# Kernel optimization log

Measured on AMD Instinct MI355X. Metric: run time of the kernel, lower is better.

## Reference

```python
import jax, jax.numpy as jnp
import numpy as np

CH = [32, 64, 128, 256, 512]
# per decoder stage s (s=0 deepest): conv_a Cin = CH[3-s] + in_ch, Cout = CH[3-s]; conv_b CH[3-s]->CH[3-s]
STAGE_DIMS = [(768, 256), (384, 128), (192, 64), (96, 32)]


def three_interpolation(p1, p2, x2):
    """p1 [B,N1,3] dense coords, p2 [B,N2,3] sparse coords, x2 [B,C,N2] -> [B,C,N1]."""
    d2 = (jnp.sum(p1 * p1, -1)[:, :, None]
          - 2.0 * jnp.einsum('bnd,bmd->bnm', p1, p2)
          + jnp.sum(p2 * p2, -1)[:, None, :])            # [B,N1,N2] squared dists
    neg_d, idx = jax.lax.top_k(-d2, 3)                   # 3 nearest neighbors
    dist = jnp.maximum(-neg_d, 0.0)                      # [B,N1,3]
    w = 1.0 / (dist + 1e-8)
    w = w / jnp.sum(w, axis=-1, keepdims=True)           # inverse-distance weights
    gathered = jax.vmap(lambda x, i: x[:, i])(x2, idx)   # [B,C,N1,3]
    return jnp.einsum('bcnk,bnk->bcn', gathered, w)


def conv_bn_relu(x, W, g, b):
    # 1x1 conv1d + BN (eval: running mean 0, var 1) + ReLU
    y = jnp.einsum('oc,bcn->bon', W, x)
    return jax.nn.relu(y * g[None, :, None] + b[None, :, None])


def setup_inputs() -> dict:
    key = jax.random.key(0)
    B = 8
    Ns = [8192, 2048, 512, 128, 32]
    inp = {}
    keys = jax.random.split(key, 64)
    ki = 0
    for i, n in enumerate(Ns):
        inp[f'p{i}'] = jax.random.uniform(keys[ki], (B, n, 3), jnp.float32); ki += 1
        inp[f'f{i}'] = jax.random.normal(keys[ki], (B, CH[i], n), jnp.float32); ki += 1
    for s, (cin, cout) in enumerate(STAGE_DIMS):
        inp[f'w{s}a'] = jax.random.normal(keys[ki], (cout, cin), jnp.float32) * 0.05; ki += 1
        inp[f'g{s}a'] = 1.0 + 0.1 * jax.random.normal(keys[ki], (cout,), jnp.float32); ki += 1
        inp[f'b{s}a'] = 0.1 * jax.random.normal(keys[ki], (cout,), jnp.float32); ki += 1
        inp[f'w{s}b'] = jax.random.normal(keys[ki], (cout, cout), jnp.float32) * 0.05; ki += 1
        inp[f'g{s}b'] = 1.0 + 0.1 * jax.random.normal(keys[ki], (cout,), jnp.float32); ki += 1
        inp[f'b{s}b'] = 0.1 * jax.random.normal(keys[ki], (cout,), jnp.float32); ki += 1
    return inp


def reference(p0, p1, p2, p3, p4, f0, f1, f2, f3, f4,
              w0a, g0a, b0a, w0b, g0b, b0b,
              w1a, g1a, b1a, w1b, g1b, b1b,
              w2a, g2a, b2a, w2b, g2b, b2b,
              w3a, g3a, b3a, w3b, g3b, b3b):
    p = [p0, p1, p2, p3, p4]
    f = [f0, f1, f2, f3, f4]
    params = [(w0a, g0a, b0a, w0b, g0b, b0b),
              (w1a, g1a, b1a, w1b, g1b, b1b),
              (w2a, g2a, b2a, w2b, g2b, b2b),
              (w3a, g3a, b3a, w3b, g3b, b3b)]
    # decoder stage s propagates level (4-s) -> (3-s)
    for s in range(4):
        lvl = 3 - s
        interp = three_interpolation(p[lvl], p[lvl + 1], f[lvl + 1])
        x = jnp.concatenate([f[lvl], interp], axis=1)
        wa, ga, ba, wb, gb, bb = params[s]
        x = conv_bn_relu(x, wa, ga, ba)
        x = conv_bn_relu(x, wb, gb, bb)
        f[lvl] = x
    return f[0]
```

## Files before the change

kernel.cpp:

```cpp
#include <hip/hip_runtime.h>

#define KNN_INF 3.0e38f
#define GD 8
#define NCELL 512
#define H 0.125f


__global__ __launch_bounds__(512) void bin_kernel(const float* __restrict__ p2,
                                                  float4* __restrict__ bpts,
                                                  int* __restrict__ bidx,
                                                  int* __restrict__ cstart,
                                                  int N2) {
    __shared__ int cnt[NCELL], cnt0[NCELL], cur[NCELL];
    __shared__ int cellof[2048];
    int b = blockIdx.x;
    int t = threadIdx.x;
    cnt[t] = 0;
    __syncthreads();
    float xs[4], ys[4], zs[4];
    for (int i = 0; i < 4; ++i) {
        int m = t * 4 + i;
        const float* q = p2 + ((size_t)b * N2 + m) * 3;
        float x = q[0], y = q[1], z = q[2];
        xs[i] = x; ys[i] = y; zs[i] = z;
        int ix = min(GD - 1, max(0, (int)(x * 8.0f)));
        int iy = min(GD - 1, max(0, (int)(y * 8.0f)));
        int iz = min(GD - 1, max(0, (int)(z * 8.0f)));
        int c = (ix << 6) | (iy << 3) | iz;
        cellof[m] = c;
        atomicAdd(&cnt[c], 1);
    }
    __syncthreads();
    int myc = cnt[t];
    cnt0[t] = myc;
    __syncthreads();
    for (int off = 1; off < NCELL; off <<= 1) {
        int v = (t >= off) ? cnt[t - off] : 0;
        __syncthreads();
        cnt[t] += v;
        __syncthreads();
    }
    int excl = cnt[t] - cnt0[t];
    cur[t] = excl;
    cstart[b * (NCELL + 1) + t] = excl;
    if (t == 0) cstart[b * (NCELL + 1) + NCELL] = N2;
    __syncthreads();
    for (int i = 0; i < 4; ++i) {
        int m = t * 4 + i;
        int c = cellof[m];
        int pos = atomicAdd(&cur[c], 1);
        float x = xs[i], y = ys[i], z = zs[i];
        bpts[(size_t)b * N2 + pos] = make_float4(x, y, z, x * x + y * y + z * z);
        bidx[(size_t)b * N2 + pos] = m;
    }
}

__device__ __forceinline__ bool lex_lt(float da, int ia, float db, int ib) {
    return (da < db) || (da == db && ia < ib);
}

__global__ __launch_bounds__(256) void knn_query_kernel(
    const float* __restrict__ p1,
    const float4* __restrict__ bpts,
    const int* __restrict__ bidx,
    const int* __restrict__ cstart,
    int* __restrict__ idx, float* __restrict__ w,
    int N1, int N2) {
    int n = blockIdx.x * 256 + threadIdx.x;
    int b = blockIdx.y;
    if (n >= N1) return;
    const float* pp = p1 + ((size_t)b * N1 + n) * 3;
    float px = pp[0], py = pp[1], pz = pp[2];
    float s1 = px * px + py * py + pz * pz;
    int cx = min(GD - 1, max(0, (int)(px * 8.0f)));
    int cy = min(GD - 1, max(0, (int)(py * 8.0f)));
    int cz = min(GD - 1, max(0, (int)(pz * 8.0f)));
    float d0 = KNN_INF, d1 = KNN_INF, d2 = KNN_INF;
    int i0 = 0, i1 = 0, i2 = 0;
    const float4* bp = bpts + (size_t)b * N2;
    const int* bi = bidx + (size_t)b * N2;
    const int* cs = cstart + b * (NCELL + 1);

#define SCAN_CELL(ci, cj, ck)                                            \
    {                                                                    \
        int c_ = ((ci) << 6) | ((cj) << 3) | (ck);                       \
        int e_ = cs[c_ + 1];                                             \
        for (int m_ = cs[c_]; m_ < e_; ++m_) {                           \
            float4 q = bp[m_];                                           \
            int om = bi[m_];                                             \
            float dot = px * q.x + py * q.y + pz * q.z;                  \
            float d = fmaf(-2.0f, dot, s1 + q.w);                        \
            if (lex_lt(d, om, d2, i2)) {                                 \
                if (lex_lt(d, om, d1, i1)) {                             \
                    d2 = d1; i2 = i1;                                    \
                    if (lex_lt(d, om, d0, i0)) {                         \
                        d1 = d0; i1 = i0; d0 = d; i0 = om;               \
                    } else { d1 = d; i1 = om; }                          \
                } else { d2 = d; i2 = om; }                              \
            }                                                            \
        }                                                                \
    }

    int x0 = max(cx - 1, 0), x1 = min(cx + 1, GD - 1);
    int y0 = max(cy - 1, 0), y1 = min(cy + 1, GD - 1);
    int z0 = max(cz - 1, 0), z1 = min(cz + 1, GD - 1);
    for (int i = x0; i <= x1; ++i)
        for (int j = y0; j <= y1; ++j)
            for (int k = z0; k <= z1; ++k)
                SCAN_CELL(i, j, k);

    int r = 1;
    while (true) {
        float mL = (cx - r > 0)      ? (px - (float)(cx - r) * H)     : KNN_INF;
        float mR = (cx + r < GD - 1) ? ((float)(cx + r + 1) * H - px) : KNN_INF;
        float mD = (cy - r > 0)      ? (py - (float)(cy - r) * H)     : KNN_INF;
        float mU = (cy + r < GD - 1) ? ((float)(cy + r + 1) * H - py) : KNN_INF;
        float mB = (cz - r > 0)      ? (pz - (float)(cz - r) * H)     : KNN_INF;
        float mF = (cz + r < GD - 1) ? ((float)(cz + r + 1) * H - pz) : KNN_INF;
        float mg = fminf(fminf(fminf(mL, mR), fminf(mD, mU)), fminf(mB, mF));
        if (mg >= 1.0e18f) break;
        if (d2 <= mg * mg * 0.99999f) break;
        int nx0 = max(cx - r - 1, 0), nx1 = min(cx + r + 1, GD - 1);
        int ny0 = max(cy - r - 1, 0), ny1 = min(cy + r + 1, GD - 1);
        int nz0 = max(cz - r - 1, 0), nz1 = min(cz + r + 1, GD - 1);
        for (int i = nx0; i <= nx1; ++i)
            for (int j = ny0; j <= ny1; ++j)
                for (int k = nz0; k <= nz1; ++k) {
                    if (i >= x0 && i <= x1 && j >= y0 && j <= y1 && k >= z0 && k <= z1)
                        continue;
                    SCAN_CELL(i, j, k);
                }
        x0 = nx0; x1 = nx1; y0 = ny0; y1 = ny1; z0 = nz0; z1 = nz1;
        ++r;
    }
#undef SCAN_CELL

    float dd0 = fmaxf(d0, 0.0f), dd1 = fmaxf(d1, 0.0f), dd2 = fmaxf(d2, 0.0f);
    float w0 = 1.0f / (dd0 + 1e-8f);
    float w1 = 1.0f / (dd1 + 1e-8f);
    float w2 = 1.0f / (dd2 + 1e-8f);
    float wsum = w0 + w1 + w2;
    w0 /= wsum; w1 /= wsum; w2 /= wsum;
    size_t ob = ((size_t)b * N1 + n) * 3;
    idx[ob + 0] = i0; idx[ob + 1] = i1; idx[ob + 2] = i2;
    w[ob + 0] = w0; w[ob + 1] = w1; w[ob + 2] = w2;
}

struct KnnAll {
    const float* p1[3]; const float* p2[3];
    float* pd[3]; int* pi[3];
    int N1[3], N2[3], chunk[3], nchunk[3], nbx[3];
    int bs1, bs2;
};

__global__ void knn_all_kernel(KnnAll P) {
    __shared__ float4 sm4[256];
    int bid = blockIdx.x;
    int s = (bid >= P.bs1) + (bid >= P.bs2);
    int start = (s == 0) ? 0 : (s == 1) ? P.bs1 : P.bs2;
    int local = bid - start;
    int nbx = P.nbx[s];
    int bx = local % nbx;
    int rest = local / nbx;
    int b = rest & 7;
    int z = rest >> 3;
    int N1 = P.N1[s], N2 = P.N2[s], chunk = P.chunk[s], nchunk = P.nchunk[s];
    int m0 = z * chunk;
    const float* p2b = P.p2[s] + ((size_t)b * N2 + m0) * 3;
    for (int m = threadIdx.x; m < chunk; m += blockDim.x) {
        float x = p2b[m * 3 + 0], y = p2b[m * 3 + 1], zz = p2b[m * 3 + 2];
        sm4[m] = make_float4(x, y, zz, x * x + y * y + zz * zz);
    }
    __syncthreads();
    int n = bx * blockDim.x + threadIdx.x;
    if (n >= N1) return;
    const float* p1b = P.p1[s] + ((size_t)b * N1 + n) * 3;
    float px = p1b[0], py = p1b[1], pz = p1b[2];
    float s1 = px * px + py * py + pz * pz;
    float d0 = KNN_INF, d1 = KNN_INF, d2 = KNN_INF;
    int i0 = 0, i1 = 0, i2 = 0;
    for (int m = 0; m < chunk; ++m) {
        float4 q = sm4[m];
        float dot = px * q.x + py * q.y + pz * q.z;
        float d = fmaf(-2.0f, dot, s1 + q.w);
        if (d < d2) {
            if (d < d1) {
                d2 = d1; i2 = i1;
                if (d < d0) { d1 = d0; i1 = i0; d0 = d; i0 = m; }
                else        { d1 = d;  i1 = m; }
            } else { d2 = d; i2 = m; }
        }
    }
    size_t base = (((size_t)b * N1 + n) * nchunk + z) * 3;
    float* pd = P.pd[s]; int* pi = P.pi[s];
    pd[base + 0] = d0; pd[base + 1] = d1; pd[base + 2] = d2;
    pi[base + 0] = m0 + i0; pi[base + 1] = m0 + i1; pi[base + 2] = m0 + i2;
}

struct MergeAll {
    const float* pd[3]; const int* pi[3];
    int* idx[3]; float* w[3];
    int nchunk[3];
    int ts1, ts2;
};

__global__ void knn_merge_all_kernel(MergeAll P, int total) {
    int t = blockIdx.x * blockDim.x + threadIdx.x;
    if (t >= total) return;
    int s = (t >= P.ts1) + (t >= P.ts2);
    int start = (s == 0) ? 0 : (s == 1) ? P.ts1 : P.ts2;
    int lt = t - start;
    int nchunk = P.nchunk[s];
    float d0 = KNN_INF, d1 = KNN_INF, d2 = KNN_INF;
    int i0 = 0, i1 = 0, i2 = 0;
    const float* pd = P.pd[s]; const int* pi = P.pi[s];
    size_t base = (size_t)lt * nchunk * 3;
    for (int c = 0; c < nchunk * 3; ++c) {
        float d = pd[base + c];
        int   i = pi[base + c];
        if (d < d2) {
            if (d < d1) {
                d2 = d1; i2 = i1;
                if (d < d0) { d1 = d0; i1 = i0; d0 = d; i0 = i; }
                else        { d1 = d;  i1 = i; }
            } else { d2 = d; i2 = i; }
        }
    }
    float dd0 = fmaxf(d0, 0.0f), dd1 = fmaxf(d1, 0.0f), dd2 = fmaxf(d2, 0.0f);
    float w0 = 1.0f / (dd0 + 1e-8f);
    float w1 = 1.0f / (dd1 + 1e-8f);
    float w2 = 1.0f / (dd2 + 1e-8f);
    float wsum = w0 + w1 + w2;
    w0 /= wsum; w1 /= wsum; w2 /= wsum;
    size_t ob = (size_t)lt * 3;
    P.idx[s][ob + 0] = i0; P.idx[s][ob + 1] = i1; P.idx[s][ob + 2] = i2;
    P.w[s][ob + 0] = w0; P.w[s][ob + 1] = w1; P.w[s][ob + 2] = w2;
}

#define TO 32
#define TN 64
#define BK 16
template<bool PARTIAL>
__global__ __launch_bounds__(256) void conv_a_fused_kernel(
    const float* __restrict__ f1, const float* __restrict__ x2,
    const int* __restrict__ idxS, const float* __restrict__ wS,
    const float* __restrict__ W, const float* __restrict__ g, const float* __restrict__ bv,
    float* __restrict__ Y,
    int C1, int C2, int N, int N2, int Cout, int chunk) {
    __shared__ float Ws[BK][TO];
    __shared__ float Xs[BK][TN];
    int Cin = C1 + C2;
    int zb = blockIdx.z;
    int b = zb & 7;
    int split = zb >> 3;
    int kBase = split * chunk;
    int oBase = blockIdx.y * TO;
    int nBase = blockIdx.x * TN;
    int tid = threadIdx.x;
    int tx = tid & 15;
    int ty = tid >> 4;
    int nn = tid & 63;
    int kk0 = tid >> 6;
    int n = nBase + nn;
    size_t gb = ((size_t)b * N + n) * 3;
    int j0 = idxS[gb + 0], j1 = idxS[gb + 1], j2 = idxS[gb + 2];
    float w0g = wS[gb + 0], w1g = wS[gb + 1], w2g = wS[gb + 2];
    const float* f1b = f1 + (size_t)b * C1 * N;
    const float* x2b = x2 + (size_t)b * C2 * N2;
    float acc[2][4] = {{0.f, 0.f, 0.f, 0.f}, {0.f, 0.f, 0.f, 0.f}};
    for (int k0 = kBase; k0 < kBase + chunk; k0 += BK) {
        for (int t = tid; t < TO * BK; t += 256) {
            int o = t / BK, kk = t % BK;
            Ws[kk][o] = W[(size_t)(oBase + o) * Cin + k0 + kk];
        }
#pragma unroll
        for (int i = 0; i < 4; ++i) {
            int kk = kk0 + i * 4;
            int k = k0 + kk;
            float v;
            if (k < C1) {
                v = f1b[(size_t)k * N + n];
            } else {
                const float* r = x2b + (size_t)(k - C1) * N2;
                v = r[j0] * w0g + r[j1] * w1g + r[j2] * w2g;
            }
            Xs[kk][nn] = v;
        }
        __syncthreads();
#pragma unroll
        for (int kk = 0; kk < BK; ++kk) {
            float w0 = Ws[kk][ty * 2 + 0];
            float w1 = Ws[kk][ty * 2 + 1];
            float4 xv = *reinterpret_cast<const float4*>(&Xs[kk][tx * 4]);
            acc[0][0] = fmaf(w0, xv.x, acc[0][0]);
            acc[0][1] = fmaf(w0, xv.y, acc[0][1]);
            acc[0][2] = fmaf(w0, xv.z, acc[0][2]);
            acc[0][3] = fmaf(w0, xv.w, acc[0][3]);
            acc[1][0] = fmaf(w1, xv.x, acc[1][0]);
            acc[1][1] = fmaf(w1, xv.y, acc[1][1]);
            acc[1][2] = fmaf(w1, xv.z, acc[1][2]);
            acc[1][3] = fmaf(w1, xv.w, acc[1][3]);
        }
        __syncthreads();
    }
#pragma unroll
    for (int r = 0; r < 2; ++r) {
        int o = oBase + ty * 2 + r;
        float4 st;
        if (PARTIAL) {
            st.x = acc[r][0]; st.y = acc[r][1]; st.z = acc[r][2]; st.w = acc[r][3];
            *reinterpret_cast<float4*>(&Y[((size_t)zb * Cout + o) * N + nBase + tx * 4]) = st;
        } else {
            float gg = g[o], bb = bv[o];
            st.x = fmaxf(fmaf(acc[r][0], gg, bb), 0.0f);
            st.y = fmaxf(fmaf(acc[r][1], gg, bb), 0.0f);
            st.z = fmaxf(fmaf(acc[r][2], gg, bb), 0.0f);
            st.w = fmaxf(fmaf(acc[r][3], gg, bb), 0.0f);
            *reinterpret_cast<float4*>(&Y[((size_t)b * Cout + o) * N + nBase + tx * 4]) = st;
        }
    }
}

template<bool PARTIAL>
__global__ __launch_bounds__(256) void conv_gemm_kernel(
    const float* __restrict__ X, const float* __restrict__ W,
    const float* __restrict__ g, const float* __restrict__ bv,
    float* __restrict__ Y, int Cin, int Cout, int N, int chunk) {
    __shared__ float Ws[BK][TO];
    __shared__ float Xs[BK][TN];
    int zb = blockIdx.z;
    int b = zb & 7;
    int split = zb >> 3;
    int kBase = split * chunk;
    int oBase = blockIdx.y * TO;
    int nBase = blockIdx.x * TN;
    int tid = threadIdx.x;
    int tx = tid & 15;
    int ty = tid >> 4;
    float acc[2][4] = {{0.f, 0.f, 0.f, 0.f}, {0.f, 0.f, 0.f, 0.f}};
    const float* Xb = X + (size_t)b * Cin * N;
    for (int k0 = kBase; k0 < kBase + chunk; k0 += BK) {
        for (int t = tid; t < TO * BK; t += 256) {
            int o = t / BK, kk = t % BK;
            Ws[kk][o] = W[(size_t)(oBase + o) * Cin + k0 + kk];
        }
        for (int t = tid; t < BK * TN; t += 256) {
            int kk = t / TN, nnn = t % TN;
            Xs[kk][nnn] = Xb[(size_t)(k0 + kk) * N + nBase + nnn];
        }
        __syncthreads();
#pragma unroll
        for (int kk = 0; kk < BK; ++kk) {
            float w0 = Ws[kk][ty * 2 + 0];
            float w1 = Ws[kk][ty * 2 + 1];
            float4 xv = *reinterpret_cast<const float4*>(&Xs[kk][tx * 4]);
            acc[0][0] = fmaf(w0, xv.x, acc[0][0]);
            acc[0][1] = fmaf(w0, xv.y, acc[0][1]);
            acc[0][2] = fmaf(w0, xv.z, acc[0][2]);
            acc[0][3] = fmaf(w0, xv.w, acc[0][3]);
            acc[1][0] = fmaf(w1, xv.x, acc[1][0]);
            acc[1][1] = fmaf(w1, xv.y, acc[1][1]);
            acc[1][2] = fmaf(w1, xv.z, acc[1][2]);
            acc[1][3] = fmaf(w1, xv.w, acc[1][3]);
        }
        __syncthreads();
    }
#pragma unroll
    for (int r = 0; r < 2; ++r) {
        int o = oBase + ty * 2 + r;
        float4 st;
        if (PARTIAL) {
            st.x = acc[r][0]; st.y = acc[r][1]; st.z = acc[r][2]; st.w = acc[r][3];
            *reinterpret_cast<float4*>(&Y[((size_t)zb * Cout + o) * N + nBase + tx * 4]) = st;
        } else {
            float gg = g[o], bb = bv[o];
            st.x = fmaxf(fmaf(acc[r][0], gg, bb), 0.0f);
            st.y = fmaxf(fmaf(acc[r][1], gg, bb), 0.0f);
            st.z = fmaxf(fmaf(acc[r][2], gg, bb), 0.0f);
            st.w = fmaxf(fmaf(acc[r][3], gg, bb), 0.0f);
            *reinterpret_cast<float4*>(&Y[((size_t)b * Cout + o) * N + nBase + tx * 4]) = st;
        }
    }
}

__global__ void reduce_bn_relu_kernel(const float* __restrict__ part,
                                      const float* __restrict__ g,
                                      const float* __restrict__ bv,
                                      float* __restrict__ Y,
                                      int Cout, int N, int total4, int nsplit, int stride4) {
    int t = blockIdx.x * blockDim.x + threadIdx.x;
    if (t >= total4) return;
    const float4* p4 = reinterpret_cast<const float4*>(part);
    float4 a = p4[t];
    for (int s = 1; s < nsplit; ++s) {
        float4 v = p4[t + (size_t)s * stride4];
        a.x += v.x; a.y += v.y; a.z += v.z; a.w += v.w;
    }
    int o = ((t * 4) / N) % Cout;
    float gg = g[o], bb = bv[o];
    float4 st;
    st.x = fmaxf(fmaf(a.x, gg, bb), 0.0f);
    st.y = fmaxf(fmaf(a.y, gg, bb), 0.0f);
    st.z = fmaxf(fmaf(a.z, gg, bb), 0.0f);
    st.w = fmaxf(fmaf(a.w, gg, bb), 0.0f);
    reinterpret_cast<float4*>(Y)[t] = st;
}

extern "C" void kernel_launch(void* const* d_in, const int* in_sizes, int n_in,
                              void* d_out, int out_size, void* d_ws, size_t ws_size,
                              hipStream_t stream) {
    const int B = 8;
    const int Ns[5]  = {8192, 2048, 512, 128, 32};
    const int CHs[5] = {32, 64, 128, 256, 512};

    const float* p[5];
    const float* f[5];
    for (int i = 0; i < 5; ++i) {
        p[i] = (const float*)d_in[2 * i];
        f[i] = (const float*)d_in[2 * i + 1];
    }

    int N1s[4], N2s[4], C1s[4], C2s[4];
    for (int s = 0; s < 4; ++s) {
        int lvl = 3 - s;
        N1s[s] = Ns[lvl]; N2s[s] = Ns[lvl + 1];
        C1s[s] = CHs[lvl];
        C2s[s] = (s == 0) ? CHs[4] : CHs[lvl + 1];
    }
    const int nchunks[3] = {1, 4, 8};
    int chunks[3], nbxs[3];
    for (int s = 0; s < 3; ++s) {
        chunks[s] = N2s[s] / nchunks[s];
        nbxs[s] = (N1s[s] + 255) / 256;
    }

    float* ws = (float*)d_ws;
    int*   knn_idx = (int*)ws;
    float* knn_w   = ws + 262144;
    float* part_d  = ws + 524288;
    int*   part_i  = (int*)(ws + 969728);
    float* bufA    = ws + 1415168;
    float* out0    = ws + 3512320;
    float* out1    = ws + 3774464;
    float* out2    = ws + 4298752;
    float* gpart   = ws + 5347328;
    float4* bin_pts = (float4*)(ws + 9541632);
    int*   bin_idx  = (int*)(ws + 9672704);
    int*   cell_st  = (int*)(ws + 9689088);
    float* outs[4] = {out0, out1, out2, (float*)d_out};

    int idxOff[4], pOff[3];
    {
        int a = 0;
        for (int s = 0; s < 4; ++s) { idxOff[s] = a; a += B * N1s[s] * 3; }
        int q = 0;
        for (int s = 0; s < 3; ++s) { pOff[s] = q; q += B * N1s[s] * nchunks[s] * 3; }
    }

    bin_kernel<<<B, 512, 0, stream>>>(p[1], bin_pts, bin_idx, cell_st, N2s[3]);
    {
        dim3 qg(N1s[3] / 256, B);
        knn_query_kernel<<<qg, 256, 0, stream>>>(p[0], bin_pts, bin_idx, cell_st,
                                                 knn_idx + idxOff[3], knn_w + idxOff[3],
                                                 N1s[3], N2s[3]);
    }

    KnnAll KP;
    int blk = 0;
    int bsArr[3];
    for (int s = 0; s < 3; ++s) {
        KP.p1[s] = p[3 - s]; KP.p2[s] = p[4 - s];
        KP.pd[s] = part_d + pOff[s]; KP.pi[s] = part_i + pOff[s];
        KP.N1[s] = N1s[s]; KP.N2[s] = N2s[s];
        KP.chunk[s] = chunks[s]; KP.nchunk[s] = nchunks[s]; KP.nbx[s] = nbxs[s];
        bsArr[s] = blk;
        blk += nbxs[s] * B * nchunks[s];
    }
    KP.bs1 = bsArr[1]; KP.bs2 = bsArr[2];
    knn_all_kernel<<<blk, 256, 0, stream>>>(KP);

    MergeAll MP;
    int tt = 0;
    int tsArr[3];
    for (int s = 0; s < 3; ++s) {
        MP.pd[s] = part_d + pOff[s]; MP.pi[s] = part_i + pOff[s];
        MP.idx[s] = knn_idx + idxOff[s]; MP.w[s] = knn_w + idxOff[s];
        MP.nchunk[s] = nchunks[s];
        tsArr[s] = tt;
        tt += B * N1s[s];
    }
    MP.ts1 = tsArr[1]; MP.ts2 = tsArr[2];
    knn_merge_all_kernel<<<(tt + 255) / 256, 256, 0, stream>>>(MP, tt);

    const int nsA[4] = {12, 6, 4, 1};
    const int nsB[4] = {8, 4, 2, 1};

    for (int s = 0; s < 4; ++s) {
        int N1 = N1s[s], N2 = N2s[s];
        int C1 = C1s[s], C2 = C2s[s];
        int Cin = C1 + C2, Cout = C1;
        const float* x2 = (s == 0) ? f[4] : outs[s - 1];
        const float* wa = (const float*)d_in[10 + s * 6 + 0];
        const float* ga = (const float*)d_in[10 + s * 6 + 1];
        const float* ba = (const float*)d_in[10 + s * 6 + 2];
        const float* wb = (const float*)d_in[10 + s * 6 + 3];
        const float* gb = (const float*)d_in[10 + s * 6 + 4];
        const float* bb = (const float*)d_in[10 + s * 6 + 5];
        const int* idxS = knn_idx + idxOff[s];
        const float* wSb = knn_w + idxOff[s];

        {
            int nsplit = nsA[s];
            int chunk = Cin / nsplit;
            dim3 grid(N1 / TN, Cout / TO, B * nsplit);
            if (nsplit == 1) {
                conv_a_fused_kernel<false><<<grid, 256, 0, stream>>>(
                    f[3 - s], x2, idxS, wSb, wa, ga, ba, bufA, C1, C2, N1, N2, Cout, chunk);
            } else {
                conv_a_fused_kernel<true><<<grid, 256, 0, stream>>>(
                    f[3 - s], x2, idxS, wSb, wa, ga, ba, gpart, C1, C2, N1, N2, Cout, chunk);
                int total4 = B * Cout * N1 / 4;
                reduce_bn_relu_kernel<<<(total4 + 255) / 256, 256, 0, stream>>>(
                    gpart, ga, ba, bufA, Cout, N1, total4, nsplit, total4);
            }
        }
        {
            int nsplit = nsB[s];
            int chunk = Cout / nsplit;
            dim3 grid(N1 / TN, Cout / TO, B * nsplit);
            if (nsplit == 1) {
                conv_gemm_kernel<false><<<grid, 256, 0, stream>>>(
                    bufA, wb, gb, bb, outs[s], Cout, Cout, N1, chunk);
            } else {
                conv_gemm_kernel<true><<<grid, 256, 0, stream>>>(
                    bufA, wb, gb, bb, gpart, Cout, Cout, N1, chunk);
                int total4 = B * Cout * N1 / 4;
                reduce_bn_relu_kernel<<<(total4 + 255) / 256, 256, 0, stream>>>(
                    gpart, gb, bb, outs[s], Cout, N1, total4, nsplit, total4);
            }
        }
    }
}
```

Before: 271.5 us.

## Split grid kNN query across 8 lanes per point with shuffle merge

The binned kNN query for the finest level now assigns 8 threads per query point. The lanes divide the candidate cells round-robin, and each lane's top-3 is merged with xor-shuffles before every stopping check. Cell start offsets are cached in shared memory, and the split-K factors for the conv stages are halved. The aim is more parallelism and less divergence in the serial cell scan, paid for with shuffle-merge overhead and fewer split-K partitions in the convs.

```diff
diff --git a/kernel.cpp b/kernel.cpp
--- a/kernel.cpp
+++ b/kernel.cpp
@@ -59,6 +59,18 @@
     return (da < db) || (da == db && ia < ib);
 }
 
+__device__ __forceinline__ void lex_ins(float d, int i,
+                                        float& d0, int& i0, float& d1, int& i1,
+                                        float& d2, int& i2) {
+    if (lex_lt(d, i, d2, i2)) {
+        if (lex_lt(d, i, d1, i1)) {
+            d2 = d1; i2 = i1;
+            if (lex_lt(d, i, d0, i0)) { d1 = d0; i1 = i0; d0 = d; i0 = i; }
+            else { d1 = d; i1 = i; }
+        } else { d2 = d; i2 = i; }
+    }
+}
+
 __global__ __launch_bounds__(256) void knn_query_kernel(
     const float* __restrict__ p1,
     const float4* __restrict__ bpts,
@@ -66,9 +78,14 @@
     const int* __restrict__ cstart,
     int* __restrict__ idx, float* __restrict__ w,
     int N1, int N2) {
-    int n = blockIdx.x * 256 + threadIdx.x;
+    __shared__ int scs[NCELL + 1];
     int b = blockIdx.y;
-    if (n >= N1) return;
+    for (int i = threadIdx.x; i < NCELL + 1; i += 256)
+        scs[i] = cstart[b * (NCELL + 1) + i];
+    __syncthreads();
+
+    int qlane = threadIdx.x & 7;
+    int n = blockIdx.x * 32 + (threadIdx.x >> 3);
     const float* pp = p1 + ((size_t)b * N1 + n) * 3;
     float px = pp[0], py = pp[1], pz = pp[2];
     float s1 = px * px + py * py + pz * pz;
@@ -79,38 +96,45 @@
     int i0 = 0, i1 = 0, i2 = 0;
     const float4* bp = bpts + (size_t)b * N2;
     const int* bi = bidx + (size_t)b * N2;
-    const int* cs = cstart + b * (NCELL + 1);
 
 #define SCAN_CELL(ci, cj, ck)                                            \
     {                                                                    \
         int c_ = ((ci) << 6) | ((cj) << 3) | (ck);                       \
-        int e_ = cs[c_ + 1];                                             \
-        for (int m_ = cs[c_]; m_ < e_; ++m_) {                           \
+        int e_ = scs[c_ + 1];                                            \
+        for (int m_ = scs[c_]; m_ < e_; ++m_) {                          \
             float4 q = bp[m_];                                           \
             int om = bi[m_];                                             \
             float dot = px * q.x + py * q.y + pz * q.z;                  \
             float d = fmaf(-2.0f, dot, s1 + q.w);                        \
-            if (lex_lt(d, om, d2, i2)) {                                 \
-                if (lex_lt(d, om, d1, i1)) {                             \
-                    d2 = d1; i2 = i1;                                    \
-                    if (lex_lt(d, om, d0, i0)) {                         \
-                        d1 = d0; i1 = i0; d0 = d; i0 = om;               \
-                    } else { d1 = d; i1 = om; }                          \
-                } else { d2 = d; i2 = om; }                              \
-            }                                                            \
+            lex_ins(d, om, d0, i0, d1, i1, d2, i2);                      \
         }                                                                \
     }
 
     int x0 = max(cx - 1, 0), x1 = min(cx + 1, GD - 1);
     int y0 = max(cy - 1, 0), y1 = min(cy + 1, GD - 1);
     int z0 = max(cz - 1, 0), z1 = min(cz + 1, GD - 1);
-    for (int i = x0; i <= x1; ++i)
-        for (int j = y0; j <= y1; ++j)
-            for (int k = z0; k <= z1; ++k)
-                SCAN_CELL(i, j, k);
-
+    {
+        int t = 0;
+        for (int i = x0; i <= x1; ++i)
+            for (int j = y0; j <= y1; ++j)
+                for (int k = z0; k <= z1; ++k) {
+                    if ((t & 7) == qlane) SCAN_CELL(i, j, k);
+                    ++t;
+                }
+    }
+
+    float e0, e1, e2; int j0, j1, j2;
     int r = 1;
     while (true) {
+        e0 = d0; e1 = d1; e2 = d2; j0 = i0; j1 = i1; j2 = i2;
+#pragma unroll
+        for (int m = 1; m < 8; m <<= 1) {
+            float o0 = __shfl_xor(e0, m), o1 = __shfl_xor(e1, m), o2 = __shfl_xor(e2, m);
+            int   q0 = __shfl_xor(j0, m), q1 = __shfl_xor(j1, m), q2 = __shfl_xor(j2, m);
+            lex_ins(o0, q0, e0, j0, e1, j1, e2, j2);
+            lex_ins(o1, q1, e0, j0, e1, j1, e2, j2);
+            lex_ins(o2, q2, e0, j0, e1, j1, e2, j2);
+        }
         float mL = (cx - r > 0)      ? (px - (float)(cx - r) * H)     : KNN_INF;
         float mR = (cx + r < GD - 1) ? ((float)(cx + r + 1) * H - px) : KNN_INF;
         float mD = (cy - r > 0)      ? (py - (float)(cy - r) * H)     : KNN_INF;
@@ -119,31 +143,35 @@
         float mF = (cz + r < GD - 1) ? ((float)(cz + r + 1) * H - pz) : KNN_INF;
         float mg = fminf(fminf(fminf(mL, mR), fminf(mD, mU)), fminf(mB, mF));
         if (mg >= 1.0e18f) break;
-        if (d2 <= mg * mg * 0.99999f) break;
+        if (e2 <= mg * mg * 0.99999f) break;
         int nx0 = max(cx - r - 1, 0), nx1 = min(cx + r + 1, GD - 1);
         int ny0 = max(cy - r - 1, 0), ny1 = min(cy + r + 1, GD - 1);
         int nz0 = max(cz - r - 1, 0), nz1 = min(cz + r + 1, GD - 1);
+        int t = 0;
         for (int i = nx0; i <= nx1; ++i)
             for (int j = ny0; j <= ny1; ++j)
                 for (int k = nz0; k <= nz1; ++k) {
                     if (i >= x0 && i <= x1 && j >= y0 && j <= y1 && k >= z0 && k <= z1)
                         continue;
-                    SCAN_CELL(i, j, k);
+                    if ((t & 7) == qlane) SCAN_CELL(i, j, k);
+                    ++t;
                 }
         x0 = nx0; x1 = nx1; y0 = ny0; y1 = ny1; z0 = nz0; z1 = nz1;
         ++r;
     }
 #undef SCAN_CELL
 
-    float dd0 = fmaxf(d0, 0.0f), dd1 = fmaxf(d1, 0.0f), dd2 = fmaxf(d2, 0.0f);
-    float w0 = 1.0f / (dd0 + 1e-8f);
-    float w1 = 1.0f / (dd1 + 1e-8f);
-    float w2 = 1.0f / (dd2 + 1e-8f);
-    float wsum = w0 + w1 + w2;
-    w0 /= wsum; w1 /= wsum; w2 /= wsum;
-    size_t ob = ((size_t)b * N1 + n) * 3;
-    idx[ob + 0] = i0; idx[ob + 1] = i1; idx[ob + 2] = i2;
-    w[ob + 0] = w0; w[ob + 1] = w1; w[ob + 2] = w2;
+    if (qlane == 0) {
+        float dd0 = fmaxf(e0, 0.0f), dd1 = fmaxf(e1, 0.0f), dd2 = fmaxf(e2, 0.0f);
+        float w0 = 1.0f / (dd0 + 1e-8f);
+        float w1 = 1.0f / (dd1 + 1e-8f);
+        float w2 = 1.0f / (dd2 + 1e-8f);
+        float wsum = w0 + w1 + w2;
+        w0 /= wsum; w1 /= wsum; w2 /= wsum;
+        size_t ob = ((size_t)b * N1 + n) * 3;
+        idx[ob + 0] = j0; idx[ob + 1] = j1; idx[ob + 2] = j2;
+        w[ob + 0] = w0; w[ob + 1] = w1; w[ob + 2] = w2;
+    }
 }
 
 struct KnnAll {
@@ -459,7 +487,7 @@
 
     bin_kernel<<<B, 512, 0, stream>>>(p[1], bin_pts, bin_idx, cell_st, N2s[3]);
     {
-        dim3 qg(N1s[3] / 256, B);
+        dim3 qg(N1s[3] / 32, B);
         knn_query_kernel<<<qg, 256, 0, stream>>>(p[0], bin_pts, bin_idx, cell_st,
                                                  knn_idx + idxOff[3], knn_w + idxOff[3],
                                                  N1s[3], N2s[3]);
@@ -492,8 +520,8 @@
     MP.ts1 = tsArr[1]; MP.ts2 = tsArr[2];
     knn_merge_all_kernel<<<(tt + 255) / 256, 256, 0, stream>>>(MP, tt);
 
-    const int nsA[4] = {12, 6, 4, 1};
-    const int nsB[4] = {8, 4, 2, 1};
+    const int nsA[4] = {6, 3, 2, 1};
+    const int nsB[4] = {4, 2, 1, 1};
 
     for (int s = 0; s < 4; ++s) {
         int N1 = N1s[s], N2 = N2s[s];
```

New measurement: 522.5 us. 92.5% more time.
